# Optimization experiments

Hardware: AMD Instinct MI355X
Metric: run time of the kernel (lower is better)

## Reference

```python
import jax, jax.numpy as jnp
import numpy as np

E, K = 8, 2
B, S, H = 8, 2048, 512
R0, R1, O = 256, 256, 512
T = B * S


def _make_routing(key):
    # Mixtral-style: top-k softmax weights [T, K] and one-hot mask [E, K, T]
    k1, k2 = jax.random.split(key)
    sel = jax.random.randint(k1, (T, K), 0, E)                      # selected expert per (token, slot)
    rw = jax.nn.softmax(jax.random.normal(k2, (T, K)), axis=-1)
    mask = jax.nn.one_hot(sel, E, dtype=jnp.bool_)                  # [T, K, E]
    mask = jnp.transpose(mask, (2, 1, 0))                           # [E, K, T]
    return mask, rw


def setup_inputs() -> dict:
    key = jax.random.key(0)
    ks = jax.random.split(key, 10)
    x = jax.random.normal(ks[0], (B, S, H), dtype=jnp.float32)
    m1, rw1 = _make_routing(ks[1])
    m2, rw2 = _make_routing(ks[2])
    m3, rw3 = _make_routing(ks[3])
    s = 0.02
    W1 = jax.random.normal(ks[4], (E, R0, H), dtype=jnp.float32) * s
    b1 = jnp.zeros((E, R0), dtype=jnp.float32)
    W2 = jax.random.normal(ks[5], (E, R1, R0), dtype=jnp.float32) * s
    b2 = jnp.zeros((E, R1), dtype=jnp.float32)
    W3 = jax.random.normal(ks[6], (E, O, R1), dtype=jnp.float32) * s
    b3 = jnp.zeros((E, O), dtype=jnp.float32)
    return {"x": x,
            "expert_mask1": m1, "expert_mask2": m2, "expert_mask3": m3,
            "routing_weights1": rw1, "routing_weights2": rw2, "routing_weights3": rw3,
            "W1": W1, "b1": b1, "W2": W2, "b2": b2, "W3": W3, "b3": b3}


def _moe_stage(h, mask, rw, W, b, act):
    # combine[e, t] = routing weight of token t for expert e (0 if not routed)
    cmb = jnp.einsum('ekt,tk->et', mask.astype(h.dtype), rw)
    acc0 = jnp.zeros((h.shape[0], W.shape[1]), dtype=h.dtype)

    def body(acc, ew):
        Wi, bi, ci = ew            # Wi: [out, in], bi: [out], ci: [T]
        out = h @ Wi.T + bi
        if act:
            out = jax.nn.relu(out)
        return acc + ci[:, None] * out, None

    acc, _ = jax.lax.scan(body, acc0, (W, b, cmb))
    return acc


def reference(x, expert_mask1, expert_mask2, expert_mask3,
              routing_weights1, routing_weights2, routing_weights3,
              W1, b1, W2, b2, W3, b3):
    bsz, seq, dim = x.shape
    h = x.reshape(-1, dim)                                          # [T, H]
    h = _moe_stage(h, expert_mask1, routing_weights1, W1, b1, act=False)   # [T, R0]
    h = _moe_stage(h, expert_mask2, routing_weights2, W2, b2, act=False)   # [T, R1]
    h = _moe_stage(h, expert_mask3, routing_weights3, W3, b3, act=True)    # relu on expert output, then combine
    out = jax.nn.relu(h.reshape(bsz, seq, -1))
    return out
```

## Files before the change

kernel.cpp:

```cpp
#include <hip/hip_runtime.h>

#define T_TOKENS 16384
#define CAP 12288
#define CNT_STRIDE 16

typedef unsigned short u16;
typedef __attribute__((ext_vector_type(8))) short short8;
typedef __attribute__((ext_vector_type(4))) float float4v;

__device__ __forceinline__ u16 f2b(float f) {
  unsigned u = __float_as_uint(f);
  u = (u + 0x7fffu + ((u >> 16) & 1u)) >> 16;
  return (u16)u;
}
__device__ __forceinline__ float b2f(u16 h) {
  return __uint_as_float(((unsigned)h) << 16);
}

__global__ void convert_w(const float* __restrict__ W1, const float* __restrict__ W2,
                          const float* __restrict__ W3, u16* __restrict__ Wb1,
                          u16* __restrict__ Wb2, u16* __restrict__ Wb3) {
  const int n1 = 8 * 256 * 512, n2 = 8 * 256 * 256;
  int base = (blockIdx.x * 256 + threadIdx.x) * 8;
  const float* src;
  u16* dst;
  int off = base;
  if (base < n1) { src = W1; dst = Wb1; }
  else if (base < n1 + n2) { src = W2; dst = Wb2; off = base - n1; }
  else { src = W3; dst = Wb3; off = base - n1 - n2; }
  float4 a0 = *(const float4*)(src + off);
  float4 a1 = *(const float4*)(src + off + 4);
  short8 v;
  v[0] = (short)f2b(a0.x); v[1] = (short)f2b(a0.y);
  v[2] = (short)f2b(a0.z); v[3] = (short)f2b(a0.w);
  v[4] = (short)f2b(a1.x); v[5] = (short)f2b(a1.y);
  v[6] = (short)f2b(a1.z); v[7] = (short)f2b(a1.w);
  *(short8*)(dst + off) = v;
}

__global__ void route_kernel(const int* __restrict__ m1, const int* __restrict__ m2,
                             const int* __restrict__ m3, const float* __restrict__ rw1,
                             const float* __restrict__ rw2, const float* __restrict__ rw3,
                             int* __restrict__ cnt, int* __restrict__ idxbuf,
                             float* __restrict__ wgtbuf) {
  __shared__ int lcnt[24];
  __shared__ int lbase[24];
  const int tid = threadIdx.x;
  const int t = blockIdx.x * 256 + tid;
  if (tid < 24) lcnt[tid] = 0;
  __syncthreads();

  const int* masks[3] = {m1, m2, m3};
  const float* rws[3] = {rw1, rw2, rw3};
  int expert[3][2], lpos[3][2];
#pragma unroll
  for (int s = 0; s < 3; ++s)
#pragma unroll
    for (int k = 0; k < 2; ++k) {
      int e = 0;
#pragma unroll
      for (int j = 0; j < 8; ++j)
        if (masks[s][(j * 2 + k) * T_TOKENS + t] != 0) e = j;
      expert[s][k] = e;
      lpos[s][k] = atomicAdd(&lcnt[s * 8 + e], 1);
    }
  __syncthreads();
  if (tid < 24) lbase[tid] = atomicAdd(&cnt[tid * CNT_STRIDE], lcnt[tid]);
  __syncthreads();
#pragma unroll
  for (int s = 0; s < 3; ++s)
#pragma unroll
    for (int k = 0; k < 2; ++k) {
      int e = expert[s][k];
      int p = lbase[s * 8 + e] + lpos[s][k];
      if (p < CAP) {
        idxbuf[(s * 8 + e) * CAP + p] = t * 2 + k;
        wgtbuf[(s * 8 + e) * CAP + p] = rws[s][t * 2 + k];
      }
    }
}

template <int KDIM, int NDIM_TOTAL, int SRC, int RELU>
__global__ __launch_bounds__(256) void moe_gemm(
    const void* __restrict__ Asrc, const u16* __restrict__ Wb, const float* __restrict__ bias,
    const int* __restrict__ cnt, const int* __restrict__ idxbuf, const float* __restrict__ wgtbuf,
    u16* __restrict__ outTmp) {
  __shared__ __align__(16) u16 As[64][72];
  __shared__ __align__(16) u16 Bs[256][72];
  __shared__ int rowTok[64];
  __shared__ float rowW[64];

  const int e = blockIdx.y;
  const int n_e = cnt[e * CNT_STRIDE];
  const int row0 = blockIdx.x * 64;
  if (row0 >= n_e) return;
  const int nbase = blockIdx.z * 256;
  const int tid = threadIdx.x;

  if (tid < 64) {
    int g = row0 + tid;
    if (g < n_e) {
      rowTok[tid] = idxbuf[e * CAP + g];
      rowW[tid] = wgtbuf[e * CAP + g];
    } else {
      rowTok[tid] = 0;
      rowW[tid] = 0.f;
    }
  }
  __syncthreads();

  const int wave = tid >> 6, lane = tid & 63;
  const int lrow = lane & 15, lquad = lane >> 4;
  const int arow = tid >> 3;
  const int acol = (tid & 7) * 8;

  float4v acc[4][4];
#pragma unroll
  for (int i = 0; i < 4; ++i)
#pragma unroll
    for (int j = 0; j < 4; ++j) acc[i][j] = (float4v)0.f;

  const u16* Wbe = Wb + ((size_t)e * NDIM_TOTAL + nbase) * KDIM;

  for (int kb = 0; kb < KDIM; kb += 64) {
#pragma unroll
    for (int it = 0; it < 2; ++it) {
      int r = arow + it * 32;
      int tok = rowTok[r];
      short8 v;
      if (SRC == 0) {
        const float* xp = (const float*)Asrc + (size_t)(tok >> 1) * KDIM + kb + acol;
        float4 a0 = *(const float4*)xp;
        float4 a1 = *(const float4*)(xp + 4);
        v[0] = (short)f2b(a0.x); v[1] = (short)f2b(a0.y);
        v[2] = (short)f2b(a0.z); v[3] = (short)f2b(a0.w);
        v[4] = (short)f2b(a1.x); v[5] = (short)f2b(a1.y);
        v[6] = (short)f2b(a1.z); v[7] = (short)f2b(a1.w);
      } else {
        const u16* p0 = (const u16*)Asrc + ((size_t)(tok >> 1) * 2) * KDIM + kb + acol;
        short8 v0 = *(const short8*)p0;
        short8 v1 = *(const short8*)(p0 + KDIM);
#pragma unroll
        for (int j = 0; j < 8; ++j)
          v[j] = (short)f2b(b2f((u16)v0[j]) + b2f((u16)v1[j]));
      }
      *(short8*)&As[r][acol] = v;
    }
#pragma unroll
    for (int it = 0; it < 8; ++it) {
      int r = arow + it * 32;
      *(short8*)&Bs[r][acol] = *(const short8*)(Wbe + (size_t)r * KDIM + kb + acol);
    }
    __syncthreads();
#pragma unroll
    for (int ks = 0; ks < 64; ks += 32) {
      short8 af[4], bfr[4];
#pragma unroll
      for (int mt = 0; mt < 4; ++mt)
        af[mt] = *(const short8*)&As[mt * 16 + lrow][ks + lquad * 8];
#pragma unroll
      for (int nt = 0; nt < 4; ++nt)
        bfr[nt] = *(const short8*)&Bs[wave * 64 + nt * 16 + lrow][ks + lquad * 8];
#pragma unroll
      for (int mt = 0; mt < 4; ++mt)
#pragma unroll
        for (int nt = 0; nt < 4; ++nt)
          acc[mt][nt] = __builtin_amdgcn_mfma_f32_16x16x32_bf16(af[mt], bfr[nt], acc[mt][nt], 0, 0, 0);
    }
    __syncthreads();
  }

  float bv[4];
#pragma unroll
  for (int nt = 0; nt < 4; ++nt)
    bv[nt] = bias[e * NDIM_TOTAL + nbase + wave * 64 + nt * 16 + lrow];
#pragma unroll
  for (int mt = 0; mt < 4; ++mt) {
#pragma unroll
    for (int i = 0; i < 4; ++i) {
      int m = mt * 16 + lquad * 4 + i;
      if (row0 + m < n_e) {
        float w = rowW[m];
        size_t drow = (size_t)rowTok[m] * NDIM_TOTAL + nbase;
#pragma unroll
        for (int nt = 0; nt < 4; ++nt) {
          float v = acc[mt][nt][i] + bv[nt];
          if (RELU) v = fmaxf(v, 0.f);
          v *= w;
          outTmp[drow + wave * 64 + nt * 16 + lrow] = f2b(v);
        }
      }
    }
  }
}

__global__ void finalize_kernel(const u16* __restrict__ tmp3, float* __restrict__ out) {
  int f = (blockIdx.x * 256 + threadIdx.x) * 8;
  int t = f >> 9;
  int o = f & 511;
  const u16* p = tmp3 + (size_t)t * 1024 + o;
  short8 v0 = *(const short8*)p;
  short8 v1 = *(const short8*)(p + 512);
  float4 r0, r1;
  r0.x = fmaxf(b2f((u16)v0[0]) + b2f((u16)v1[0]), 0.f);
  r0.y = fmaxf(b2f((u16)v0[1]) + b2f((u16)v1[1]), 0.f);
  r0.z = fmaxf(b2f((u16)v0[2]) + b2f((u16)v1[2]), 0.f);
  r0.w = fmaxf(b2f((u16)v0[3]) + b2f((u16)v1[3]), 0.f);
  r1.x = fmaxf(b2f((u16)v0[4]) + b2f((u16)v1[4]), 0.f);
  r1.y = fmaxf(b2f((u16)v0[5]) + b2f((u16)v1[5]), 0.f);
  r1.z = fmaxf(b2f((u16)v0[6]) + b2f((u16)v1[6]), 0.f);
  r1.w = fmaxf(b2f((u16)v0[7]) + b2f((u16)v1[7]), 0.f);
  *(float4*)(out + f) = r0;
  *(float4*)(out + f + 4) = r1;
}

extern "C" void kernel_launch(void* const* d_in, const int* in_sizes, int n_in,
                              void* d_out, int out_size, void* d_ws, size_t ws_size,
                              hipStream_t stream) {
  const float* x  = (const float*)d_in[0];
  const int* m1   = (const int*)d_in[1];
  const int* m2   = (const int*)d_in[2];
  const int* m3   = (const int*)d_in[3];
  const float* rw1 = (const float*)d_in[4];
  const float* rw2 = (const float*)d_in[5];
  const float* rw3 = (const float*)d_in[6];
  const float* W1 = (const float*)d_in[7];
  const float* b1 = (const float*)d_in[8];
  const float* W2 = (const float*)d_in[9];
  const float* b2 = (const float*)d_in[10];
  const float* W3 = (const float*)d_in[11];
  const float* b3 = (const float*)d_in[12];
  float* out = (float*)d_out;

  char* ws = (char*)d_ws;
  size_t off = 0;
  int* cnt = (int*)(ws + off); off += 24 * CNT_STRIDE * 4;
  u16* Wb1 = (u16*)(ws + off); off += (size_t)8 * 256 * 512 * 2;
  u16* Wb2 = (u16*)(ws + off); off += (size_t)8 * 256 * 256 * 2;
  u16* Wb3 = (u16*)(ws + off); off += (size_t)8 * 512 * 256 * 2;
  u16* tmp1 = (u16*)(ws + off); off += (size_t)T_TOKENS * 2 * 256 * 2;
  u16* tmp2 = (u16*)(ws + off); off += (size_t)T_TOKENS * 2 * 256 * 2;
  u16* tmp3 = (u16*)(ws + off); off += (size_t)T_TOKENS * 2 * 512 * 2;
  int* idxb = (int*)(ws + off); off += (size_t)3 * 8 * CAP * 4;
  float* wgtb = (float*)(ws + off); off += (size_t)3 * 8 * CAP * 4;

  hipMemsetAsync(cnt, 0, 24 * CNT_STRIDE * 4, stream);
  convert_w<<<1280, 256, 0, stream>>>(W1, W2, W3, Wb1, Wb2, Wb3);
  route_kernel<<<64, 256, 0, stream>>>(m1, m2, m3, rw1, rw2, rw3, cnt, idxb, wgtb);

  moe_gemm<512, 256, 0, 0><<<dim3(CAP / 64, 8, 1), 256, 0, stream>>>(
      x, Wb1, b1, cnt + 0, idxb + 0, wgtb + 0, tmp1);
  moe_gemm<256, 256, 1, 0><<<dim3(CAP / 64, 8, 1), 256, 0, stream>>>(
      tmp1, Wb2, b2, cnt + 8 * CNT_STRIDE, idxb + 8 * CAP, wgtb + 8 * CAP, tmp2);
  moe_gemm<256, 512, 1, 1><<<dim3(CAP / 64, 8, 2), 256, 0, stream>>>(
      tmp2, Wb3, b3, cnt + 16 * CNT_STRIDE, idxb + 16 * CAP, wgtb + 16 * CAP, tmp3);

  finalize_kernel<<<4096, 256, 0, stream>>>(tmp3, out);
}
```

Baseline: 192.1 us.

## Compact expert grid, 128-row tiles, direct global-to-LDS loads with swizzle

Pre-converts x to bf16 along with the weights in a single kernel, which also zeroes the counters and so removes the memset. The GEMM now maps a flat block index onto per-expert 128-row tiles, so no blocks are launched only to exit. Each block computes a 128x256 tile with a 2x2 wave layout and 4x8 MFMA accumulators. B (and A in stage 1) are loaded with global_load_lds into an XOR-swizzled LDS layout. The aim is to cut wasted blocks, per-thread staging work and LDS bank conflicts, at the cost of higher register pressure and fewer resident blocks per CU.

```diff
diff --git a/kernel.cpp b/kernel.cpp
--- a/kernel.cpp
+++ b/kernel.cpp
@@ -5,6 +5,7 @@
 #define CNT_STRIDE 16
 
 typedef unsigned short u16;
+typedef unsigned int u32;
 typedef __attribute__((ext_vector_type(8))) short short8;
 typedef __attribute__((ext_vector_type(4))) float float4v;
 
@@ -17,17 +18,24 @@
   return __uint_as_float(((unsigned)h) << 16);
 }
 
-__global__ void convert_w(const float* __restrict__ W1, const float* __restrict__ W2,
-                          const float* __restrict__ W3, u16* __restrict__ Wb1,
-                          u16* __restrict__ Wb2, u16* __restrict__ Wb3) {
-  const int n1 = 8 * 256 * 512, n2 = 8 * 256 * 256;
+__device__ __forceinline__ void gl_lds16(const u16* g, u16* l) {
+  __builtin_amdgcn_global_load_lds((const __attribute__((address_space(1))) u32*)g,
+                                   (__attribute__((address_space(3))) u32*)l, 16, 0, 0);
+}
+
+__global__ void convert_all(const float* __restrict__ x, const float* __restrict__ W1,
+                            const float* __restrict__ W2, const float* __restrict__ W3,
+                            u16* __restrict__ xb, u16* __restrict__ Wb1,
+                            u16* __restrict__ Wb2, u16* __restrict__ Wb3,
+                            int* __restrict__ cnt) {
+  if (blockIdx.x == 0 && threadIdx.x < 24) cnt[threadIdx.x * CNT_STRIDE] = 0;
+  const int nx = T_TOKENS * 512, n1 = 8 * 256 * 512, n2 = 8 * 256 * 256;
   int base = (blockIdx.x * 256 + threadIdx.x) * 8;
-  const float* src;
-  u16* dst;
-  int off = base;
-  if (base < n1) { src = W1; dst = Wb1; }
-  else if (base < n1 + n2) { src = W2; dst = Wb2; off = base - n1; }
-  else { src = W3; dst = Wb3; off = base - n1 - n2; }
+  const float* src; u16* dst; int off = base;
+  if (base < nx) { src = x; dst = xb; }
+  else if (base < nx + n1) { src = W1; dst = Wb1; off = base - nx; }
+  else if (base < nx + n1 + n2) { src = W2; dst = Wb2; off = base - nx - n1; }
+  else { src = W3; dst = Wb3; off = base - nx - n1 - n2; }
   float4 a0 = *(const float4*)(src + off);
   float4 a1 = *(const float4*)(src + off + 4);
   short8 v;
@@ -81,117 +89,139 @@
 }
 
 template <int KDIM, int NDIM_TOTAL, int SRC, int RELU>
-__global__ __launch_bounds__(256) void moe_gemm(
-    const void* __restrict__ Asrc, const u16* __restrict__ Wb, const float* __restrict__ bias,
+__global__ __launch_bounds__(256, 2) void moe_gemm(
+    const u16* __restrict__ Asrc, const u16* __restrict__ Wb, const float* __restrict__ bias,
     const int* __restrict__ cnt, const int* __restrict__ idxbuf, const float* __restrict__ wgtbuf,
     u16* __restrict__ outTmp) {
-  __shared__ __align__(16) u16 As[64][72];
-  __shared__ __align__(16) u16 Bs[256][72];
-  __shared__ int rowTok[64];
-  __shared__ float rowW[64];
-
-  const int e = blockIdx.y;
-  const int n_e = cnt[e * CNT_STRIDE];
-  const int row0 = blockIdx.x * 64;
-  if (row0 >= n_e) return;
-  const int nbase = blockIdx.z * 256;
+  __shared__ __align__(16) u16 As[128 * 64];
+  __shared__ __align__(16) u16 Bs[256 * 64];
+  __shared__ int rowTok[128];
+  __shared__ float rowW[128];
+
+  int b = blockIdx.x;
+  int e = -1, row0 = 0, n_e = 0, accb = 0;
+#pragma unroll
+  for (int j = 0; j < 8; ++j) {
+    int nj = cnt[j * CNT_STRIDE];
+    nj = nj > CAP ? CAP : nj;
+    int nb = (nj + 127) >> 7;
+    if (e < 0 && b < accb + nb) { e = j; row0 = (b - accb) << 7; n_e = nj; }
+    accb += nb;
+  }
+  if (e < 0) return;
+
   const int tid = threadIdx.x;
-
-  if (tid < 64) {
+  if (tid < 128) {
     int g = row0 + tid;
-    if (g < n_e) {
-      rowTok[tid] = idxbuf[e * CAP + g];
-      rowW[tid] = wgtbuf[e * CAP + g];
+    bool ok = g < n_e;
+    rowTok[tid] = ok ? idxbuf[e * CAP + g] : 0;
+    rowW[tid] = ok ? wgtbuf[e * CAP + g] : 0.f;
+  }
+  __syncthreads();
+
+  const int nbase = blockIdx.y * 256;
+  const int wv = tid >> 6, lane = tid & 63;
+  const int lrow = lane & 15, lquad = lane >> 4;
+  const int mh = wv >> 1, nh = wv & 1;
+
+  const u16* Wbe = Wb + ((size_t)e * NDIM_TOTAL + nbase) * KDIM;
+
+  const int lr = lane >> 3;
+  const int lgl = (lane & 7) ^ lr;
+  const u16* gB = Wbe + (size_t)(wv * 8 + lr) * KDIM + lgl * 8;
+  u16* lB = &Bs[(wv * 8) * 64];
+  u16* lA = &As[(wv * 8) * 64];
+
+  const u16* gA[4];
+  const u16* ga0[4];
+  int awoff[4];
+  if (SRC == 0) {
+#pragma unroll
+    for (int i = 0; i < 4; ++i) {
+      int r = i * 32 + wv * 8 + lr;
+      gA[i] = Asrc + (size_t)(rowTok[r] >> 1) * KDIM + lgl * 8;
+    }
+  } else {
+#pragma unroll
+    for (int i = 0; i < 4; ++i) {
+      int r = i * 32 + (tid >> 3);
+      ga0[i] = Asrc + (size_t)(rowTok[r] >> 1) * 2 * KDIM + (tid & 7) * 8;
+      awoff[i] = (r * 8 + ((tid & 7) ^ ((tid >> 3) & 7))) * 8;
+    }
+  }
+
+  float4v acc[4][8];
+#pragma unroll
+  for (int mt = 0; mt < 4; ++mt)
+#pragma unroll
+    for (int nt = 0; nt < 8; ++nt) acc[mt][nt] = (float4v)0.f;
+
+  for (int kb = 0; kb < KDIM; kb += 64) {
+#pragma unroll
+    for (int i = 0; i < 8; ++i)
+      gl_lds16(gB + (size_t)i * 32 * KDIM + kb, lB + i * 32 * 64);
+    if (SRC == 0) {
+#pragma unroll
+      for (int i = 0; i < 4; ++i)
+        gl_lds16(gA[i] + kb, lA + i * 32 * 64);
     } else {
-      rowTok[tid] = 0;
-      rowW[tid] = 0.f;
-    }
-  }
-  __syncthreads();
-
-  const int wave = tid >> 6, lane = tid & 63;
-  const int lrow = lane & 15, lquad = lane >> 4;
-  const int arow = tid >> 3;
-  const int acol = (tid & 7) * 8;
-
-  float4v acc[4][4];
-#pragma unroll
-  for (int i = 0; i < 4; ++i)
-#pragma unroll
-    for (int j = 0; j < 4; ++j) acc[i][j] = (float4v)0.f;
-
-  const u16* Wbe = Wb + ((size_t)e * NDIM_TOTAL + nbase) * KDIM;
-
-  for (int kb = 0; kb < KDIM; kb += 64) {
-#pragma unroll
-    for (int it = 0; it < 2; ++it) {
-      int r = arow + it * 32;
-      int tok = rowTok[r];
-      short8 v;
-      if (SRC == 0) {
-        const float* xp = (const float*)Asrc + (size_t)(tok >> 1) * KDIM + kb + acol;
-        float4 a0 = *(const float4*)xp;
-        float4 a1 = *(const float4*)(xp + 4);
-        v[0] = (short)f2b(a0.x); v[1] = (short)f2b(a0.y);
-        v[2] = (short)f2b(a0.z); v[3] = (short)f2b(a0.w);
-        v[4] = (short)f2b(a1.x); v[5] = (short)f2b(a1.y);
-        v[6] = (short)f2b(a1.z); v[7] = (short)f2b(a1.w);
-      } else {
-        const u16* p0 = (const u16*)Asrc + ((size_t)(tok >> 1) * 2) * KDIM + kb + acol;
-        short8 v0 = *(const short8*)p0;
-        short8 v1 = *(const short8*)(p0 + KDIM);
+#pragma unroll
+      for (int i = 0; i < 4; ++i) {
+        short8 v0 = *(const short8*)(ga0[i] + kb);
+        short8 v1 = *(const short8*)(ga0[i] + kb + KDIM);
+        short8 v;
 #pragma unroll
         for (int j = 0; j < 8; ++j)
           v[j] = (short)f2b(b2f((u16)v0[j]) + b2f((u16)v1[j]));
-      }
-      *(short8*)&As[r][acol] = v;
-    }
-#pragma unroll
-    for (int it = 0; it < 8; ++it) {
-      int r = arow + it * 32;
-      *(short8*)&Bs[r][acol] = *(const short8*)(Wbe + (size_t)r * KDIM + kb + acol);
+        *(short8*)&As[awoff[i]] = v;
+      }
     }
     __syncthreads();
 #pragma unroll
     for (int ks = 0; ks < 64; ks += 32) {
-      short8 af[4], bfr[4];
+      const int gb = ks >> 3;
+      short8 af[4], bf[8];
+#pragma unroll
+      for (int mt = 0; mt < 4; ++mt) {
+        int r = mh * 64 + mt * 16 + lrow;
+        int p = (gb + lquad) ^ (lrow & 7);
+        af[mt] = *(const short8*)&As[(r * 8 + p) * 8];
+      }
+#pragma unroll
+      for (int nt = 0; nt < 8; ++nt) {
+        int r = nh * 128 + nt * 16 + lrow;
+        int p = (gb + lquad) ^ (lrow & 7);
+        bf[nt] = *(const short8*)&Bs[(r * 8 + p) * 8];
+      }
 #pragma unroll
       for (int mt = 0; mt < 4; ++mt)
-        af[mt] = *(const short8*)&As[mt * 16 + lrow][ks + lquad * 8];
-#pragma unroll
-      for (int nt = 0; nt < 4; ++nt)
-        bfr[nt] = *(const short8*)&Bs[wave * 64 + nt * 16 + lrow][ks + lquad * 8];
-#pragma unroll
-      for (int mt = 0; mt < 4; ++mt)
-#pragma unroll
-        for (int nt = 0; nt < 4; ++nt)
-          acc[mt][nt] = __builtin_amdgcn_mfma_f32_16x16x32_bf16(af[mt], bfr[nt], acc[mt][nt], 0, 0, 0);
+#pragma unroll
+        for (int nt = 0; nt < 8; ++nt)
+          acc[mt][nt] = __builtin_amdgcn_mfma_f32_16x16x32_bf16(af[mt], bf[nt], acc[mt][nt], 0, 0, 0);
     }
     __syncthreads();
   }
 
-  float bv[4];
-#pragma unroll
-  for (int nt = 0; nt < 4; ++nt)
-    bv[nt] = bias[e * NDIM_TOTAL + nbase + wave * 64 + nt * 16 + lrow];
-#pragma unroll
-  for (int mt = 0; mt < 4; ++mt) {
+  float bv[8];
+#pragma unroll
+  for (int nt = 0; nt < 8; ++nt)
+    bv[nt] = bias[e * NDIM_TOTAL + nbase + nh * 128 + nt * 16 + lrow];
+#pragma unroll
+  for (int mt = 0; mt < 4; ++mt)
 #pragma unroll
     for (int i = 0; i < 4; ++i) {
-      int m = mt * 16 + lquad * 4 + i;
+      int m = mh * 64 + mt * 16 + lquad * 4 + i;
       if (row0 + m < n_e) {
         float w = rowW[m];
-        size_t drow = (size_t)rowTok[m] * NDIM_TOTAL + nbase;
-#pragma unroll
-        for (int nt = 0; nt < 4; ++nt) {
+        size_t drow = (size_t)rowTok[m] * NDIM_TOTAL + nbase + nh * 128;
+#pragma unroll
+        for (int nt = 0; nt < 8; ++nt) {
           float v = acc[mt][nt][i] + bv[nt];
           if (RELU) v = fmaxf(v, 0.f);
-          v *= w;
-          outTmp[drow + wave * 64 + nt * 16 + lrow] = f2b(v);
+          outTmp[drow + nt * 16 + lrow] = f2b(v * w);
         }
       }
     }
-  }
 }
 
 __global__ void finalize_kernel(const u16* __restrict__ tmp3, float* __restrict__ out) {
@@ -235,6 +265,7 @@
   char* ws = (char*)d_ws;
   size_t off = 0;
   int* cnt = (int*)(ws + off); off += 24 * CNT_STRIDE * 4;
+  u16* xb  = (u16*)(ws + off); off += (size_t)T_TOKENS * 512 * 2;
   u16* Wb1 = (u16*)(ws + off); off += (size_t)8 * 256 * 512 * 2;
   u16* Wb2 = (u16*)(ws + off); off += (size_t)8 * 256 * 256 * 2;
   u16* Wb3 = (u16*)(ws + off); off += (size_t)8 * 512 * 256 * 2;
@@ -244,15 +275,14 @@
   int* idxb = (int*)(ws + off); off += (size_t)3 * 8 * CAP * 4;
   float* wgtb = (float*)(ws + off); off += (size_t)3 * 8 * CAP * 4;
 
-  hipMemsetAsync(cnt, 0, 24 * CNT_STRIDE * 4, stream);
-  convert_w<<<1280, 256, 0, stream>>>(W1, W2, W3, Wb1, Wb2, Wb3);
+  convert_all<<<5376, 256, 0, stream>>>(x, W1, W2, W3, xb, Wb1, Wb2, Wb3, cnt);
   route_kernel<<<64, 256, 0, stream>>>(m1, m2, m3, rw1, rw2, rw3, cnt, idxb, wgtb);
 
-  moe_gemm<512, 256, 0, 0><<<dim3(CAP / 64, 8, 1), 256, 0, stream>>>(
-      x, Wb1, b1, cnt + 0, idxb + 0, wgtb + 0, tmp1);
-  moe_gemm<256, 256, 1, 0><<<dim3(CAP / 64, 8, 1), 256, 0, stream>>>(
+  moe_gemm<512, 256, 0, 0><<<dim3(264, 1), 256, 0, stream>>>(
+      xb, Wb1, b1, cnt + 0, idxb + 0, wgtb + 0, tmp1);
+  moe_gemm<256, 256, 1, 0><<<dim3(264, 1), 256, 0, stream>>>(
       tmp1, Wb2, b2, cnt + 8 * CNT_STRIDE, idxb + 8 * CAP, wgtb + 8 * CAP, tmp2);
-  moe_gemm<256, 512, 1, 1><<<dim3(CAP / 64, 8, 2), 256, 0, stream>>>(
+  moe_gemm<256, 512, 1, 1><<<dim3(264, 2), 256, 0, stream>>>(
       tmp2, Wb3, b3, cnt + 16 * CNT_STRIDE, idxb + 16 * CAP, wgtb + 16 * CAP, tmp3);
 
   finalize_kernel<<<4096, 256, 0, stream>>>(tmp3, out);
```

Result: slower. 197.4 us (+2.7%).
